# Optimization experiments

Measured on AMD Instinct MI355X. Metric: run time of the kernel, lower is better.

The kernel has to match this reference:

```python
import jax, jax.numpy as jnp
import numpy as np

B, S, D, H = 2, 2048, 1024, 16
HD = D // H  # head_dim = 64


def setup_inputs() -> dict:
    key = jax.random.key(0)
    ks = jax.random.split(key, 5)
    scale = 0.02
    x = jax.random.normal(ks[0], (B, S, D), dtype=jnp.float32)
    Wq = scale * jax.random.normal(ks[1], (H, D, HD), dtype=jnp.float32)
    Wk = scale * jax.random.normal(ks[2], (H, D, HD), dtype=jnp.float32)
    Wv = scale * jax.random.normal(ks[3], (H, D, HD), dtype=jnp.float32)
    Wo = scale * jax.random.normal(ks[4], (D, D), dtype=jnp.float32)
    bq = jnp.zeros((H, HD), dtype=jnp.float32)
    bk = jnp.zeros((H, HD), dtype=jnp.float32)
    bv = jnp.zeros((H, HD), dtype=jnp.float32)
    bo = jnp.zeros((D,), dtype=jnp.float32)
    return {"x": x, "Wq": Wq, "bq": bq, "Wk": Wk, "bk": bk,
            "Wv": Wv, "bv": bv, "Wo": Wo, "bo": bo}


def reference(x, Wq, bq, Wk, bk, Wv, bv, Wo, bo):
    # Per-head QKV projections (the torch module's per-head nn.Linear list,
    # vectorized over the head axis h). Dropout is identity (eval mode).
    q = jnp.einsum("bsd,hde->bhse", x, Wq) + bq[None, :, None, :]  # [B,H,S,HD]
    k = jnp.einsum("bsd,hde->bhse", x, Wk) + bk[None, :, None, :]
    v = jnp.einsum("bsd,hde->bhse", x, Wv) + bv[None, :, None, :]

    norm = jnp.asarray(np.sqrt(HD), dtype=x.dtype)
    scores = jnp.einsum("bhse,bhte->bhst", q, k) / norm  # [B,H,S,S]
    causal = jnp.tril(jnp.ones((S, S), dtype=bool))
    scores = jnp.where(causal[None, None], scores, jnp.asarray(-jnp.inf, dtype=scores.dtype))
    attn = jax.nn.softmax(scores, axis=-1)

    wv = jnp.einsum("bhst,bhte->bhse", attn, v)          # [B,H,S,HD]
    wv = jnp.transpose(wv, (0, 2, 1, 3)).reshape(B, S, D)  # concat heads on last dim
    out = wv @ Wo.T + bo                                   # output projection
    return out
```

## Files before the change

### kernel.cpp

```cpp
#include <hip/hip_runtime.h>


#define DD 1024
#define SS 2048
#define BB 2
#define HH 16
#define HD 64
#define QSCALE 0.18033688011112042f

typedef __attribute__((ext_vector_type(8))) short short8;
typedef __attribute__((ext_vector_type(4))) float float4v;
typedef unsigned short ushort;
typedef unsigned int uint;

__device__ inline ushort f2bf(float f) {
    union { float f; uint i; } v; v.f = f;
    uint r = v.i + 0x7FFF + ((v.i >> 16) & 1);
    return (ushort)(r >> 16);
}
#if __has_builtin(__builtin_amdgcn_cvt_pk_bf16_f32)
typedef __bf16 bf16x2 __attribute__((ext_vector_type(2)));
__device__ inline uint pack_bf2(float a, float b) {
    union { bf16x2 v; uint u; } c;
    c.v = __builtin_amdgcn_cvt_pk_bf16_f32(a, b);
    return c.u;
}
#else
__device__ inline uint pack_bf2(float a, float b) {
    union { float f; uint i; } x, y; x.f = a; y.f = b;
    return ((x.i + 0x8000u) >> 16) | (((y.i + 0x8000u) >> 16) << 16);
}
#endif

__device__ __forceinline__ void cp16(const ushort* g, ushort* l) {
    __builtin_amdgcn_global_load_lds((const __attribute__((address_space(1))) void*)g,
                                     (__attribute__((address_space(3))) void*)l,
                                     16, 0, 0);
}

__global__ __launch_bounds__(256) void prep(const float* __restrict__ x,
                                            const float* __restrict__ Wo,
                                            const float* __restrict__ Wq,
                                            const float* __restrict__ Wk,
                                            const float* __restrict__ Wv,
                                            ushort* __restrict__ xb,
                                            ushort* __restrict__ Wob,
                                            ushort* __restrict__ W3T) {
    __shared__ ushort T[64][65];
    int bid = blockIdx.x, t = threadIdx.x;
    if (bid < 5120) {
        const float* src; ushort* dst; int j;
        if (bid < 4096) { src = x;  dst = xb;  j = bid * 256 + t; }
        else            { src = Wo; dst = Wob; j = (bid - 4096) * 256 + t; }
        float4 v = ((const float4*)src)[j];
        ushort o[4] = { f2bf(v.x), f2bf(v.y), f2bf(v.z), f2bf(v.w) };
        ((uint2*)dst)[j] = *(const uint2*)o;
        return;
    }
    int i = bid - 5120;
    int z = i >> 8, h = (i >> 4) & 15, d0 = (i & 15) * 64;
    const float* W = z == 0 ? Wq : (z == 1 ? Wk : Wv);
    const float* Wh = W + h * DD * HD;
    ushort* Wt = W3T + ((size_t)z * HH + h) * HD * DD;
    #pragma unroll
    for (int s = 0; s < 4; s++) {
        int idx = t + s * 256;
        int d = idx >> 4, e4 = (idx & 15) * 4;
        float4 v = *(const float4*)(Wh + (d0 + d) * HD + e4);
        T[d][e4 + 0] = f2bf(v.x); T[d][e4 + 1] = f2bf(v.y);
        T[d][e4 + 2] = f2bf(v.z); T[d][e4 + 3] = f2bf(v.w);
    }
    __syncthreads();
    #pragma unroll
    for (int s = 0; s < 2; s++) {
        int idx = t + s * 256;
        int e = idx >> 3, d8 = (idx & 7) * 8;
        ushort tmp[8];
        #pragma unroll
        for (int j = 0; j < 8; j++) tmp[j] = T[d8 + j][e];
        *(uint4*)(Wt + e * DD + d0 + d8) = *(uint4*)tmp;
    }
}

__global__ __launch_bounds__(256) void gemm_qkv(const ushort* __restrict__ xb,
                                                const ushort* __restrict__ W3T,
                                                const float* __restrict__ bq,
                                                const float* __restrict__ bk,
                                                const float* __restrict__ bv,
                                                ushort* __restrict__ qb,
                                                ushort* __restrict__ kb,
                                                ushort* __restrict__ vT) {
    __shared__ ushort Al[128 * 64];
    __shared__ ushort Bl[3][64 * 64];
    int m0 = blockIdx.x * 128, n0 = blockIdx.y * 64;
    int t = threadIdx.x, lane = t & 63, w = t >> 6;
    int wm = w & 1, wn = w >> 1;
    int qm = lane >> 4, lm = lane & 15;

    const ushort* W0 = W3T + (size_t)n0 * DD;
    const ushort* W1 = W3T + (size_t)(HH * HD + n0) * DD;
    const ushort* W2 = W3T + (size_t)(2 * HH * HD + n0) * DD;

    float4v acc[3][4][2] = {};
    for (int k0 = 0; k0 < DD; k0 += 64) {
        __syncthreads();
        #pragma unroll
        for (int s = 0; s < 4; s++) {
            int c = t + s * 256;
            int row = c >> 3;
            int j = (c & 7) ^ (row & 7);
            cp16(xb + (size_t)(m0 + row) * DD + k0 + j * 8, Al + c * 8);
        }
        #pragma unroll
        for (int s = 0; s < 2; s++) {
            int c = t + s * 256;
            int row = c >> 3;
            int j = (c & 7) ^ (row & 7);
            cp16(W0 + (size_t)row * DD + k0 + j * 8, Bl[0] + c * 8);
            cp16(W1 + (size_t)row * DD + k0 + j * 8, Bl[1] + c * 8);
            cp16(W2 + (size_t)row * DD + k0 + j * 8, Bl[2] + c * 8);
        }
        __syncthreads();
        #pragma unroll
        for (int h2 = 0; h2 < 2; h2++) {
            int sw = ((((h2 << 2) | qm) ^ (lm & 7)) << 3);
            short8 a[4];
            #pragma unroll
            for (int i = 0; i < 4; i++)
                a[i] = *(const short8*)(Al + ((wm * 64 + i * 16 + lm) << 6) + sw);
            #pragma unroll
            for (int z = 0; z < 3; z++) {
                short8 b0 = *(const short8*)(Bl[z] + ((wn * 32 + lm) << 6) + sw);
                short8 b1 = *(const short8*)(Bl[z] + ((wn * 32 + 16 + lm) << 6) + sw);
                if (z == 2) {
                    #pragma unroll
                    for (int i = 0; i < 4; i++) {
                        acc[2][i][0] = __builtin_amdgcn_mfma_f32_16x16x32_bf16(a[i], b0, acc[2][i][0], 0, 0, 0);
                        acc[2][i][1] = __builtin_amdgcn_mfma_f32_16x16x32_bf16(a[i], b1, acc[2][i][1], 0, 0, 0);
                    }
                } else {
                    #pragma unroll
                    for (int i = 0; i < 4; i++) {
                        acc[z][i][0] = __builtin_amdgcn_mfma_f32_16x16x32_bf16(b0, a[i], acc[z][i][0], 0, 0, 0);
                        acc[z][i][1] = __builtin_amdgcn_mfma_f32_16x16x32_bf16(b1, a[i], acc[z][i][1], 0, 0, 0);
                    }
                }
            }
        }
    }
    #pragma unroll
    for (int z = 0; z < 2; z++) {
        const float* bias = z == 0 ? bq : bk;
        ushort* Out = z == 0 ? qb : kb;
        float sc = z == 0 ? QSCALE : 1.0f;
        #pragma unroll
        for (int j = 0; j < 2; j++) {
            int nb = n0 + wn * 32 + j * 16 + qm * 4;
            float4 b4 = *(const float4*)(bias + nb);
            #pragma unroll
            for (int i = 0; i < 4; i++) {
                int m = m0 + wm * 64 + i * 16 + lm;
                uint2 o2;
                o2.x = pack_bf2((acc[z][i][j][0] + b4.x) * sc, (acc[z][i][j][1] + b4.y) * sc);
                o2.y = pack_bf2((acc[z][i][j][2] + b4.z) * sc, (acc[z][i][j][3] + b4.w) * sc);
                *(uint2*)(Out + (size_t)m * DD + nb) = o2;
            }
        }
    }
    #pragma unroll
    for (int j = 0; j < 2; j++) {
        int n = n0 + wn * 32 + j * 16 + lm;
        int h = n >> 6, e = n & 63;
        float bb = bv[n];
        #pragma unroll
        for (int i = 0; i < 4; i++) {
            int m = m0 + wm * 64 + i * 16 + qm * 4;
            int b_ = m >> 11, s = m & (SS - 1);
            uint2 o2;
            o2.x = pack_bf2(acc[2][i][j][0] + bb, acc[2][i][j][1] + bb);
            o2.y = pack_bf2(acc[2][i][j][2] + bb, acc[2][i][j][3] + bb);
            *(uint2*)(vT + ((size_t)(b_ * HH + h) * HD + e) * SS + s) = o2;
        }
    }
}

__global__ __launch_bounds__(256, 4) void attn(const ushort* __restrict__ Q,
                                               const ushort* __restrict__ K,
                                               const ushort* __restrict__ VT,
                                               ushort* __restrict__ O) {
    __shared__ ushort Ql[64 * 64];
    __shared__ ushort Kl[2][64 * 64];
    __shared__ ushort Vl[2][64 * 64];
    int id = blockIdx.x;
    int bh = id & 31;
    int j5 = (id >> 5) & 7;
    int quad = id >> 8;
    int qt = (quad == 0) ? (31 - j5) : (quad == 1) ? (16 + j5)
           : (quad == 2) ? (15 - j5) : j5;
    int b = bh >> 4, h = bh & 15;
    int m0 = qt * 64;
    const ushort* Qp = Q + (size_t)b * SS * DD + h * HD;
    const ushort* Kp = K + (size_t)b * SS * DD + h * HD;
    const ushort* Vp = VT + (size_t)bh * HD * SS;
    int t = threadIdx.x, lane = t & 63, w = t >> 6;
    int qm = lane >> 4, lm = lane & 15;
    int qg = m0 + w * 16 + lm;
    int swz = ((qm ^ (lm & 7)) << 3);
    int swz1 = (((4 | qm) ^ (lm & 7)) << 3);

    #pragma unroll
    for (int s2 = 0; s2 < 2; s2++) {
        int c = t + s2 * 256;
        int row = c >> 3, sj = (c & 7) ^ (row & 7);
        cp16(Qp + (size_t)(m0 + row) * DD + sj * 8, Ql + c * 8);
        cp16(Kp + (size_t)row * DD + sj * 8, Kl[0] + c * 8);
        cp16(Vp + (size_t)row * SS + sj * 8, Vl[0] + c * 8);
    }
    __syncthreads();

    short8 qf[2];
    qf[0] = *(const short8*)(Ql + ((w * 16 + lm) << 6) + swz);
    qf[1] = *(const short8*)(Ql + ((w * 16 + lm) << 6) + swz1);

    float4v o[4] = {};
    float li = 0.f;
    int cur = 0;

    for (int jt = 0; jt <= qt; jt++) {
        if (jt) __syncthreads();
        if (jt < qt) {
            int nn = (jt + 1) * 64;
            #pragma unroll
            for (int s2 = 0; s2 < 2; s2++) {
                int c = t + s2 * 256;
                int row = c >> 3, sj = (c & 7) ^ (row & 7);
                cp16(Kp + (size_t)(nn + row) * DD + sj * 8, Kl[cur ^ 1] + c * 8);
                cp16(Vp + (size_t)row * SS + nn + sj * 8, Vl[cur ^ 1] + c * 8);
            }
        }

        float4v s[4] = {};
        __builtin_amdgcn_s_setprio(1);
        #pragma unroll
        for (int j = 0; j < 4; j++) {
            short8 ak0 = *(const short8*)(Kl[cur] + ((j * 16 + lm) << 6) + swz);
            short8 ak1 = *(const short8*)(Kl[cur] + ((j * 16 + lm) << 6) + swz1);
            s[j] = __builtin_amdgcn_mfma_f32_16x16x32_bf16(ak0, qf[0], s[j], 0, 0, 0);
            s[j] = __builtin_amdgcn_mfma_f32_16x16x32_bf16(ak1, qf[1], s[j], 0, 0, 0);
        }
        __builtin_amdgcn_s_setprio(0);
        if (jt == qt) {
            #pragma unroll
            for (int j = 0; j < 4; j++)
                #pragma unroll
                for (int r = 0; r < 4; r++)
                    if (jt * 64 + j * 16 + qm * 4 + r > qg) s[j][r] = -__builtin_inff();
        }
        #pragma unroll
        for (int j = 0; j < 4; j++) {
            float p0 = __builtin_amdgcn_exp2f(s[j][0]);
            float p1 = __builtin_amdgcn_exp2f(s[j][1]);
            float p2 = __builtin_amdgcn_exp2f(s[j][2]);
            float p3 = __builtin_amdgcn_exp2f(s[j][3]);
            li += (p0 + p1) + (p2 + p3);
            uint2 u; u.x = pack_bf2(p0, p1); u.y = pack_bf2(p2, p3);
            int pc = (2 * j + (qm >> 1)) ^ (lm & 7);
            *(uint2*)(Ql + ((w * 16 + lm) << 6) + (pc << 3) + (qm & 1) * 4) = u;
        }
        asm volatile("s_waitcnt lgkmcnt(0)" ::: "memory");

        __builtin_amdgcn_s_setprio(1);
        #pragma unroll
        for (int kc = 0; kc < 2; kc++) {
            short8 ap = *(const short8*)(Ql + ((w * 16 + lm) << 6) + (kc ? swz1 : swz));
            #pragma unroll
            for (int jn = 0; jn < 4; jn++) {
                short8 av = *(const short8*)(Vl[cur] + ((jn * 16 + lm) << 6) + (kc ? swz1 : swz));
                o[jn] = __builtin_amdgcn_mfma_f32_16x16x32_bf16(av, ap, o[jn], 0, 0, 0);
            }
        }
        __builtin_amdgcn_s_setprio(0);
        cur ^= 1;
    }
    li += __shfl_xor(li, 16, 64);
    li += __shfl_xor(li, 32, 64);
    float inv = 1.f / li;
    ushort* Ob = O + ((size_t)b * SS + qg) * DD + h * HD;
    #pragma unroll
    for (int jn = 0; jn < 4; jn++) {
        uint2 u;
        u.x = pack_bf2(o[jn][0] * inv, o[jn][1] * inv);
        u.y = pack_bf2(o[jn][2] * inv, o[jn][3] * inv);
        *(uint2*)(Ob + jn * 16 + qm * 4) = u;
    }
}

__global__ __launch_bounds__(256) void gemm_out(const ushort* __restrict__ X,
                                                const ushort* __restrict__ Wob,
                                                const float* __restrict__ bo,
                                                float* __restrict__ Out) {
    __shared__ ushort Al[128 * 64];
    __shared__ ushort Bl[64 * 64];
    int m0 = blockIdx.x * 128, n0 = blockIdx.y * 64;
    int t = threadIdx.x, lane = t & 63, w = t >> 6;
    int wm = w & 1, wn = w >> 1;
    int qm = lane >> 4, lm = lane & 15;

    float4v acc[4][2] = {};
    for (int k0 = 0; k0 < DD; k0 += 64) {
        __syncthreads();
        #pragma unroll
        for (int s = 0; s < 4; s++) {
            int c = t + s * 256;
            int row = c >> 3;
            int j = (c & 7) ^ (row & 7);
            cp16(X + (size_t)(m0 + row) * DD + k0 + j * 8, Al + c * 8);
        }
        #pragma unroll
        for (int s = 0; s < 2; s++) {
            int c = t + s * 256;
            int row = c >> 3;
            int j = (c & 7) ^ (row & 7);
            cp16(Wob + (size_t)(n0 + row) * DD + k0 + j * 8, Bl + c * 8);
        }
        __syncthreads();
        #pragma unroll
        for (int h2 = 0; h2 < 2; h2++) {
            int sw = ((((h2 << 2) | qm) ^ (lm & 7)) << 3);
            short8 a[4], b[2];
            #pragma unroll
            for (int i = 0; i < 4; i++)
                a[i] = *(const short8*)(Al + ((wm * 64 + i * 16 + lm) << 6) + sw);
            #pragma unroll
            for (int j = 0; j < 2; j++)
                b[j] = *(const short8*)(Bl + ((wn * 32 + j * 16 + lm) << 6) + sw);
            #pragma unroll
            for (int i = 0; i < 4; i++)
                #pragma unroll
                for (int j = 0; j < 2; j++)
                    acc[i][j] = __builtin_amdgcn_mfma_f32_16x16x32_bf16(b[j], a[i], acc[i][j], 0, 0, 0);
        }
    }
    #pragma unroll
    for (int j = 0; j < 2; j++) {
        int nb = n0 + wn * 32 + j * 16 + qm * 4;
        float4 b4 = *(const float4*)(bo + nb);
        #pragma unroll
        for (int i = 0; i < 4; i++) {
            int m = m0 + wm * 64 + i * 16 + lm;
            float4 st;
            st.x = acc[i][j][0] + b4.x;
            st.y = acc[i][j][1] + b4.y;
            st.z = acc[i][j][2] + b4.z;
            st.w = acc[i][j][3] + b4.w;
            *(float4*)(Out + (size_t)m * DD + nb) = st;
        }
    }
}

extern "C" void kernel_launch(void* const* d_in, const int* in_sizes, int n_in,
                              void* d_out, int out_size, void* d_ws, size_t ws_size,
                              hipStream_t stream) {
    const float* x   = (const float*)d_in[0];
    const float* Wq  = (const float*)d_in[1];
    const float* bq  = (const float*)d_in[2];
    const float* Wk  = (const float*)d_in[3];
    const float* bk  = (const float*)d_in[4];
    const float* Wv_ = (const float*)d_in[5];
    const float* bv  = (const float*)d_in[6];
    const float* Wo  = (const float*)d_in[7];
    const float* bo  = (const float*)d_in[8];
    float* out = (float*)d_out;

    ushort* xb  = (ushort*)d_ws;
    ushort* W3T = xb  + (size_t)BB * SS * DD;
    ushort* Wob = W3T + (size_t)3 * HH * HD * DD;
    ushort* qb  = Wob + (size_t)DD * DD;
    ushort* kb  = qb + (size_t)BB * SS * DD;
    ushort* vT  = kb + (size_t)BB * SS * DD;
    ushort* wvb = vT + (size_t)BB * SS * DD;

    prep<<<dim3(5888), 256, 0, stream>>>(x, Wo, Wq, Wk, Wv_, xb, Wob, W3T);
    gemm_qkv<<<dim3(32, 16), 256, 0, stream>>>(xb, W3T, bq, bk, bv, qb, kb, vT);
    attn<<<dim3(1024), 256, 0, stream>>>(qb, kb, vT, wvb);
    gemm_out<<<dim3(32, 16), 256, 0, stream>>>(wvb, Wob, bo, out);
}
```

Baseline: 181.3 us.

## Process two query row groups per wave in attention, halving block threads

The attention kernel now runs 2 waves per block instead of 4. Each wave handles 32 query rows as two 16-row groups, so every K and V fragment read from shared memory feeds two MFMAs. This cuts LDS read traffic per MFMA and improves operand reuse. In exchange it uses more registers per wave (launch bounds change to 128 threads, min 2 blocks) and has fewer waves per block to hide the load and sync latency.

After: 187.7 us. 3.5% more time.

```diff
diff --git a/kernel.cpp b/kernel.cpp
--- a/kernel.cpp
+++ b/kernel.cpp
@@ -184,7 +184,7 @@
     }
 }
 
-__global__ __launch_bounds__(256, 4) void attn(const ushort* __restrict__ Q,
+__global__ __launch_bounds__(128, 2) void attn(const ushort* __restrict__ Q,
                                                const ushort* __restrict__ K,
                                                const ushort* __restrict__ VT,
                                                ushort* __restrict__ O) {
@@ -204,13 +204,12 @@
     const ushort* Vp = VT + (size_t)bh * HD * SS;
     int t = threadIdx.x, lane = t & 63, w = t >> 6;
     int qm = lane >> 4, lm = lane & 15;
-    int qg = m0 + w * 16 + lm;
     int swz = ((qm ^ (lm & 7)) << 3);
     int swz1 = (((4 | qm) ^ (lm & 7)) << 3);
 
     #pragma unroll
-    for (int s2 = 0; s2 < 2; s2++) {
-        int c = t + s2 * 256;
+    for (int s2 = 0; s2 < 4; s2++) {
+        int c = t + s2 * 128;
         int row = c >> 3, sj = (c & 7) ^ (row & 7);
         cp16(Qp + (size_t)(m0 + row) * DD + sj * 8, Ql + c * 8);
         cp16(Kp + (size_t)row * DD + sj * 8, Kl[0] + c * 8);
@@ -218,12 +217,16 @@
     }
     __syncthreads();
 
-    short8 qf[2];
-    qf[0] = *(const short8*)(Ql + ((w * 16 + lm) << 6) + swz);
-    qf[1] = *(const short8*)(Ql + ((w * 16 + lm) << 6) + swz1);
-
-    float4v o[4] = {};
-    float li = 0.f;
+    short8 qf[2][2];
+    #pragma unroll
+    for (int g = 0; g < 2; g++) {
+        int rb = (w * 32 + g * 16 + lm) << 6;
+        qf[g][0] = *(const short8*)(Ql + rb + swz);
+        qf[g][1] = *(const short8*)(Ql + rb + swz1);
+    }
+
+    float4v o[4][2] = {};
+    float li[2] = {0.f, 0.f};
     int cur = 0;
 
     for (int jt = 0; jt <= qt; jt++) {
@@ -231,67 +234,88 @@
         if (jt < qt) {
             int nn = (jt + 1) * 64;
             #pragma unroll
-            for (int s2 = 0; s2 < 2; s2++) {
-                int c = t + s2 * 256;
+            for (int s2 = 0; s2 < 4; s2++) {
+                int c = t + s2 * 128;
                 int row = c >> 3, sj = (c & 7) ^ (row & 7);
                 cp16(Kp + (size_t)(nn + row) * DD + sj * 8, Kl[cur ^ 1] + c * 8);
                 cp16(Vp + (size_t)row * SS + nn + sj * 8, Vl[cur ^ 1] + c * 8);
             }
         }
 
-        float4v s[4] = {};
+        float4v s[4][2] = {};
         __builtin_amdgcn_s_setprio(1);
         #pragma unroll
         for (int j = 0; j < 4; j++) {
             short8 ak0 = *(const short8*)(Kl[cur] + ((j * 16 + lm) << 6) + swz);
             short8 ak1 = *(const short8*)(Kl[cur] + ((j * 16 + lm) << 6) + swz1);
-            s[j] = __builtin_amdgcn_mfma_f32_16x16x32_bf16(ak0, qf[0], s[j], 0, 0, 0);
-            s[j] = __builtin_amdgcn_mfma_f32_16x16x32_bf16(ak1, qf[1], s[j], 0, 0, 0);
+            #pragma unroll
+            for (int g = 0; g < 2; g++) {
+                s[j][g] = __builtin_amdgcn_mfma_f32_16x16x32_bf16(ak0, qf[g][0], s[j][g], 0, 0, 0);
+                s[j][g] = __builtin_amdgcn_mfma_f32_16x16x32_bf16(ak1, qf[g][1], s[j][g], 0, 0, 0);
+            }
         }
         __builtin_amdgcn_s_setprio(0);
         if (jt == qt) {
             #pragma unroll
-            for (int j = 0; j < 4; j++)
+            for (int g = 0; g < 2; g++) {
+                int qg = m0 + w * 32 + g * 16 + lm;
                 #pragma unroll
-                for (int r = 0; r < 4; r++)
-                    if (jt * 64 + j * 16 + qm * 4 + r > qg) s[j][r] = -__builtin_inff();
-        }
-        #pragma unroll
-        for (int j = 0; j < 4; j++) {
-            float p0 = __builtin_amdgcn_exp2f(s[j][0]);
-            float p1 = __builtin_amdgcn_exp2f(s[j][1]);
-            float p2 = __builtin_amdgcn_exp2f(s[j][2]);
-            float p3 = __builtin_amdgcn_exp2f(s[j][3]);
-            li += (p0 + p1) + (p2 + p3);
-            uint2 u; u.x = pack_bf2(p0, p1); u.y = pack_bf2(p2, p3);
-            int pc = (2 * j + (qm >> 1)) ^ (lm & 7);
-            *(uint2*)(Ql + ((w * 16 + lm) << 6) + (pc << 3) + (qm & 1) * 4) = u;
+                for (int j = 0; j < 4; j++)
+                    #pragma unroll
+                    for (int r = 0; r < 4; r++)
+                        if (jt * 64 + j * 16 + qm * 4 + r > qg) s[j][g][r] = -__builtin_inff();
+            }
+        }
+        #pragma unroll
+        for (int g = 0; g < 2; g++) {
+            int rb = (w * 32 + g * 16 + lm) << 6;
+            #pragma unroll
+            for (int j = 0; j < 4; j++) {
+                float p0 = __builtin_amdgcn_exp2f(s[j][g][0]);
+                float p1 = __builtin_amdgcn_exp2f(s[j][g][1]);
+                float p2 = __builtin_amdgcn_exp2f(s[j][g][2]);
+                float p3 = __builtin_amdgcn_exp2f(s[j][g][3]);
+                li[g] += (p0 + p1) + (p2 + p3);
+                uint2 u; u.x = pack_bf2(p0, p1); u.y = pack_bf2(p2, p3);
+                int pc = (2 * j + (qm >> 1)) ^ (lm & 7);
+                *(uint2*)(Ql + rb + (pc << 3) + (qm & 1) * 4) = u;
+            }
         }
         asm volatile("s_waitcnt lgkmcnt(0)" ::: "memory");
 
         __builtin_amdgcn_s_setprio(1);
         #pragma unroll
         for (int kc = 0; kc < 2; kc++) {
-            short8 ap = *(const short8*)(Ql + ((w * 16 + lm) << 6) + (kc ? swz1 : swz));
+            short8 ap[2];
+            #pragma unroll
+            for (int g = 0; g < 2; g++)
+                ap[g] = *(const short8*)(Ql + ((w * 32 + g * 16 + lm) << 6) + (kc ? swz1 : swz));
             #pragma unroll
             for (int jn = 0; jn < 4; jn++) {
                 short8 av = *(const short8*)(Vl[cur] + ((jn * 16 + lm) << 6) + (kc ? swz1 : swz));
-                o[jn] = __builtin_amdgcn_mfma_f32_16x16x32_bf16(av, ap, o[jn], 0, 0, 0);
+                #pragma unroll
+                for (int g = 0; g < 2; g++)
+                    o[jn][g] = __builtin_amdgcn_mfma_f32_16x16x32_bf16(av, ap[g], o[jn][g], 0, 0, 0);
             }
         }
         __builtin_amdgcn_s_setprio(0);
         cur ^= 1;
     }
-    li += __shfl_xor(li, 16, 64);
-    li += __shfl_xor(li, 32, 64);
-    float inv = 1.f / li;
-    ushort* Ob = O + ((size_t)b * SS + qg) * DD + h * HD;
-    #pragma unroll
-    for (int jn = 0; jn < 4; jn++) {
-        uint2 u;
-        u.x = pack_bf2(o[jn][0] * inv, o[jn][1] * inv);
-        u.y = pack_bf2(o[jn][2] * inv, o[jn][3] * inv);
-        *(uint2*)(Ob + jn * 16 + qm * 4) = u;
+    #pragma unroll
+    for (int g = 0; g < 2; g++) {
+        float l = li[g];
+        l += __shfl_xor(l, 16, 64);
+        l += __shfl_xor(l, 32, 64);
+        float inv = 1.f / l;
+        int qg = m0 + w * 32 + g * 16 + lm;
+        ushort* Ob = O + ((size_t)b * SS + qg) * DD + h * HD;
+        #pragma unroll
+        for (int jn = 0; jn < 4; jn++) {
+            uint2 u;
+            u.x = pack_bf2(o[jn][g][0] * inv, o[jn][g][1] * inv);
+            u.y = pack_bf2(o[jn][g][2] * inv, o[jn][g][3] * inv);
+            *(uint2*)(Ob + jn * 16 + qm * 4) = u;
+        }
     }
 }
 
@@ -382,6 +406,6 @@
 
     prep<<<dim3(5888), 256, 0, stream>>>(x, Wo, Wq, Wk, Wv_, xb, Wob, W3T);
     gemm_qkv<<<dim3(32, 16), 256, 0, stream>>>(xb, W3T, bq, bk, bv, qb, kb, vT);
-    attn<<<dim3(1024), 256, 0, stream>>>(qb, kb, vT, wvb);
+    attn<<<dim3(1024), 128, 0, stream>>>(qb, kb, vT, wvb);
     gemm_out<<<dim3(32, 16), 256, 0, stream>>>(wvb, Wob, bo, out);
 }
```

## Rework attention with 32x32 MFMA, register-resident P, and split-KV wave pairs

Applied to the files above, without the earlier changes.

The attention kernel switches from 16x16x32 to 32x32x16 MFMA tiles. The P fragment is kept in registers via permlane32 swaps instead of being round-tripped through LDS. The two wave pairs each process alternating KV tiles, and their partial outputs and row sums are reduced through LDS at the end. This removes the LDS write/read of P and raises MFMA work per instruction. In exchange it adds a final cross-wave reduction, only half the waves do the epilogue, and the causal load balance across wave pairs becomes uneven.

Result: faster. 170.9 us, median of 2 (-5.7%).

```diff
diff --git a/kernel.cpp b/kernel.cpp
--- a/kernel.cpp
+++ b/kernel.cpp
@@ -10,6 +10,8 @@
 
 typedef __attribute__((ext_vector_type(8))) short short8;
 typedef __attribute__((ext_vector_type(4))) float float4v;
+typedef __attribute__((ext_vector_type(16))) float f32x16;
+typedef __attribute__((ext_vector_type(4))) uint uint4v;
 typedef unsigned short ushort;
 typedef unsigned int uint;
 
@@ -29,6 +31,26 @@
 __device__ inline uint pack_bf2(float a, float b) {
     union { float f; uint i; } x, y; x.f = a; y.f = b;
     return ((x.i + 0x8000u) >> 16) | (((y.i + 0x8000u) >> 16) << 16);
+}
+#endif
+
+__device__ inline short8 u4_to_s8(uint4v u) {
+    union { uint4v u; short8 s; } cv; cv.u = u; return cv.s;
+}
+
+#if __has_builtin(__builtin_amdgcn_permlane32_swap)
+typedef unsigned uint2v __attribute__((ext_vector_type(2)));
+__device__ inline void pl32_swap(uint& d, uint& s) {
+    uint2v r = __builtin_amdgcn_permlane32_swap(d, s, false, false);
+    d = r[0]; s = r[1];
+}
+#else
+__device__ inline void pl32_swap(uint& d, uint& s) {
+    uint dx = __shfl_xor(d, 32, 64), sx = __shfl_xor(s, 32, 64);
+    bool hi = (threadIdx.x & 32) != 0;
+    uint nd = hi ? sx : d;
+    uint ns = hi ? s : dx;
+    d = nd; s = ns;
 }
 #endif
 
@@ -188,9 +210,7 @@
                                                const ushort* __restrict__ K,
                                                const ushort* __restrict__ VT,
                                                ushort* __restrict__ O) {
-    __shared__ ushort Ql[64 * 64];
-    __shared__ ushort Kl[2][64 * 64];
-    __shared__ ushort Vl[2][64 * 64];
+    __shared__ ushort LB[20480];
     int id = blockIdx.x;
     int bh = id & 31;
     int j5 = (id >> 5) & 7;
@@ -203,95 +223,151 @@
     const ushort* Kp = K + (size_t)b * SS * DD + h * HD;
     const ushort* Vp = VT + (size_t)bh * HD * SS;
     int t = threadIdx.x, lane = t & 63, w = t >> 6;
-    int qm = lane >> 4, lm = lane & 15;
-    int qg = m0 + w * 16 + lm;
-    int swz = ((qm ^ (lm & 7)) << 3);
-    int swz1 = (((4 | qm) ^ (lm & 7)) << 3);
-
-    #pragma unroll
-    for (int s2 = 0; s2 < 2; s2++) {
-        int c = t + s2 * 256;
-        int row = c >> 3, sj = (c & 7) ^ (row & 7);
-        cp16(Qp + (size_t)(m0 + row) * DD + sj * 8, Ql + c * 8);
-        cp16(Kp + (size_t)row * DD + sj * 8, Kl[0] + c * 8);
-        cp16(Vp + (size_t)row * SS + sj * 8, Vl[0] + c * 8);
+    int pr = w >> 1, wq = w & 1;
+    int ln = lane & 31, hi = lane >> 5;
+    int c0 = t, c1 = t + 256;
+    int r0 = c0 >> 3, s0 = (c0 & 7) ^ (r0 & 7);
+    int r1 = c1 >> 3, s1 = (c1 & 7) ^ (r1 & 7);
+
+    cp16(Qp + (size_t)(m0 + r0) * DD + s0 * 8, LB + c0 * 8);
+    cp16(Qp + (size_t)(m0 + r1) * DD + s1 * 8, LB + c1 * 8);
+    cp16(Kp + (size_t)r0 * DD + s0 * 8, LB + 4096 + c0 * 8);
+    cp16(Kp + (size_t)r1 * DD + s1 * 8, LB + 4096 + c1 * 8);
+    cp16(Vp + (size_t)r0 * SS + s0 * 8, LB + 8192 + c0 * 8);
+    cp16(Vp + (size_t)r1 * SS + s1 * 8, LB + 8192 + c1 * 8);
+    if (qt >= 1) {
+        cp16(Kp + (size_t)(64 + r0) * DD + s0 * 8, LB + 12288 + c0 * 8);
+        cp16(Kp + (size_t)(64 + r1) * DD + s1 * 8, LB + 12288 + c1 * 8);
+        cp16(Vp + (size_t)r0 * SS + 64 + s0 * 8, LB + 16384 + c0 * 8);
+        cp16(Vp + (size_t)r1 * SS + 64 + s1 * 8, LB + 16384 + c1 * 8);
     }
     __syncthreads();
 
-    short8 qf[2];
-    qf[0] = *(const short8*)(Ql + ((w * 16 + lm) << 6) + swz);
-    qf[1] = *(const short8*)(Ql + ((w * 16 + lm) << 6) + swz1);
-
-    float4v o[4] = {};
+    short8 qf[4];
+    int qrow = wq * 32 + ln;
+    #pragma unroll
+    for (int ds_ = 0; ds_ < 4; ds_++)
+        qf[ds_] = *(const short8*)(LB + (qrow << 6) + ((((ds_ << 1) | hi) ^ (qrow & 7)) << 3));
+
+    ushort* Kb = LB + 4096 + pr * 8192;
+    ushort* Vb = LB + 8192 + pr * 8192;
+    f32x16 o[2] = {};
     float li = 0.f;
-    int cur = 0;
-
-    for (int jt = 0; jt <= qt; jt++) {
-        if (jt) __syncthreads();
-        if (jt < qt) {
-            int nn = (jt + 1) * 64;
-            #pragma unroll
-            for (int s2 = 0; s2 < 2; s2++) {
-                int c = t + s2 * 256;
-                int row = c >> 3, sj = (c & 7) ^ (row & 7);
-                cp16(Kp + (size_t)(nn + row) * DD + sj * 8, Kl[cur ^ 1] + c * 8);
-                cp16(Vp + (size_t)row * SS + nn + sj * 8, Vl[cur ^ 1] + c * 8);
-            }
-        }
-
-        float4v s[4] = {};
-        __builtin_amdgcn_s_setprio(1);
-        #pragma unroll
-        for (int j = 0; j < 4; j++) {
-            short8 ak0 = *(const short8*)(Kl[cur] + ((j * 16 + lm) << 6) + swz);
-            short8 ak1 = *(const short8*)(Kl[cur] + ((j * 16 + lm) << 6) + swz1);
-            s[j] = __builtin_amdgcn_mfma_f32_16x16x32_bf16(ak0, qf[0], s[j], 0, 0, 0);
-            s[j] = __builtin_amdgcn_mfma_f32_16x16x32_bf16(ak1, qf[1], s[j], 0, 0, 0);
-        }
-        __builtin_amdgcn_s_setprio(0);
-        if (jt == qt) {
-            #pragma unroll
-            for (int j = 0; j < 4; j++)
+    int nss = (qt + 2) >> 1;
+
+    for (int ss = 0; ss < nss; ss++) {
+        int myjt = 2 * ss + pr;
+        if (myjt <= qt) {
+            #pragma unroll
+            for (int kt = 0; kt < 2; kt++) {
+                f32x16 sacc = {};
+                __builtin_amdgcn_s_setprio(1);
                 #pragma unroll
-                for (int r = 0; r < 4; r++)
-                    if (jt * 64 + j * 16 + qm * 4 + r > qg) s[j][r] = -__builtin_inff();
-        }
-        #pragma unroll
-        for (int j = 0; j < 4; j++) {
-            float p0 = __builtin_amdgcn_exp2f(s[j][0]);
-            float p1 = __builtin_amdgcn_exp2f(s[j][1]);
-            float p2 = __builtin_amdgcn_exp2f(s[j][2]);
-            float p3 = __builtin_amdgcn_exp2f(s[j][3]);
-            li += (p0 + p1) + (p2 + p3);
-            uint2 u; u.x = pack_bf2(p0, p1); u.y = pack_bf2(p2, p3);
-            int pc = (2 * j + (qm >> 1)) ^ (lm & 7);
-            *(uint2*)(Ql + ((w * 16 + lm) << 6) + (pc << 3) + (qm & 1) * 4) = u;
-        }
-        asm volatile("s_waitcnt lgkmcnt(0)" ::: "memory");
-
-        __builtin_amdgcn_s_setprio(1);
-        #pragma unroll
-        for (int kc = 0; kc < 2; kc++) {
-            short8 ap = *(const short8*)(Ql + ((w * 16 + lm) << 6) + (kc ? swz1 : swz));
-            #pragma unroll
-            for (int jn = 0; jn < 4; jn++) {
-                short8 av = *(const short8*)(Vl[cur] + ((jn * 16 + lm) << 6) + (kc ? swz1 : swz));
-                o[jn] = __builtin_amdgcn_mfma_f32_16x16x32_bf16(av, ap, o[jn], 0, 0, 0);
-            }
-        }
-        __builtin_amdgcn_s_setprio(0);
-        cur ^= 1;
-    }
-    li += __shfl_xor(li, 16, 64);
-    li += __shfl_xor(li, 32, 64);
-    float inv = 1.f / li;
-    ushort* Ob = O + ((size_t)b * SS + qg) * DD + h * HD;
-    #pragma unroll
-    for (int jn = 0; jn < 4; jn++) {
-        uint2 u;
-        u.x = pack_bf2(o[jn][0] * inv, o[jn][1] * inv);
-        u.y = pack_bf2(o[jn][2] * inv, o[jn][3] * inv);
-        *(uint2*)(Ob + jn * 16 + qm * 4) = u;
+                for (int ds_ = 0; ds_ < 4; ds_++) {
+                    int row = kt * 32 + ln;
+                    short8 ak = *(const short8*)(Kb + (row << 6) + ((((ds_ << 1) | hi) ^ (row & 7)) << 3));
+                    sacc = __builtin_amdgcn_mfma_f32_32x32x16_bf16(ak, qf[ds_], sacc, 0, 0, 0);
+                }
+                __builtin_amdgcn_s_setprio(0);
+                if (myjt == qt) {
+                    #pragma unroll
+                    for (int r = 0; r < 16; r++) {
+                        int kk = kt * 32 + (r & 3) + 8 * (r >> 2) + 4 * hi;
+                        if (kk > qrow) sacc[r] = -__builtin_inff();
+                    }
+                }
+                float p[16];
+                #pragma unroll
+                for (int r = 0; r < 16; r++) {
+                    p[r] = __builtin_amdgcn_exp2f(sacc[r]);
+                    li += p[r];
+                }
+                uint4v pw[2];
+                #pragma unroll
+                for (int ks = 0; ks < 2; ks++) {
+                    uint c01 = pack_bf2(p[ks * 8 + 0], p[ks * 8 + 1]);
+                    uint c23 = pack_bf2(p[ks * 8 + 2], p[ks * 8 + 3]);
+                    uint c45 = pack_bf2(p[ks * 8 + 4], p[ks * 8 + 5]);
+                    uint c67 = pack_bf2(p[ks * 8 + 6], p[ks * 8 + 7]);
+                    pl32_swap(c01, c45);
+                    pl32_swap(c23, c67);
+                    uint4v pv; pv[0] = c01; pv[1] = c23; pv[2] = c45; pv[3] = c67;
+                    pw[ks] = pv;
+                }
+                __builtin_amdgcn_s_setprio(1);
+                #pragma unroll
+                for (int et = 0; et < 2; et++) {
+                    #pragma unroll
+                    for (int ks = 0; ks < 2; ks++) {
+                        int row = et * 32 + ln;
+                        int ch = ((kt << 2) | (ks << 1) | hi) ^ (row & 7);
+                        short8 av = *(const short8*)(Vb + (row << 6) + (ch << 3));
+                        o[et] = __builtin_amdgcn_mfma_f32_32x32x16_bf16(av, u4_to_s8(pw[ks]), o[et], 0, 0, 0);
+                    }
+                }
+                __builtin_amdgcn_s_setprio(0);
+            }
+        }
+        __syncthreads();
+        int nx = 2 * ss + 2;
+        if (nx <= qt) {
+            cp16(Kp + (size_t)(nx * 64 + r0) * DD + s0 * 8, LB + 4096 + c0 * 8);
+            cp16(Kp + (size_t)(nx * 64 + r1) * DD + s1 * 8, LB + 4096 + c1 * 8);
+            cp16(Vp + (size_t)r0 * SS + nx * 64 + s0 * 8, LB + 8192 + c0 * 8);
+            cp16(Vp + (size_t)r1 * SS + nx * 64 + s1 * 8, LB + 8192 + c1 * 8);
+        }
+        if (nx + 1 <= qt) {
+            cp16(Kp + (size_t)((nx + 1) * 64 + r0) * DD + s0 * 8, LB + 12288 + c0 * 8);
+            cp16(Kp + (size_t)((nx + 1) * 64 + r1) * DD + s1 * 8, LB + 12288 + c1 * 8);
+            cp16(Vp + (size_t)r0 * SS + (nx + 1) * 64 + s0 * 8, LB + 16384 + c0 * 8);
+            cp16(Vp + (size_t)r1 * SS + (nx + 1) * 64 + s1 * 8, LB + 16384 + c1 * 8);
+        }
+        __syncthreads();
+    }
+
+    float* cb = (float*)(LB + 4096);
+    float* cl = (float*)(LB + 12288);
+    if (pr == 1) {
+        float* dst = cb + ((size_t)(wq * 64 + lane)) * 32;
+        #pragma unroll
+        for (int et = 0; et < 2; et++)
+            #pragma unroll
+            for (int g2 = 0; g2 < 4; g2++) {
+                int slot = et * 4 + g2;
+                float4v v4;
+                v4[0] = o[et][g2 * 4 + 0]; v4[1] = o[et][g2 * 4 + 1];
+                v4[2] = o[et][g2 * 4 + 2]; v4[3] = o[et][g2 * 4 + 3];
+                *(float4v*)(dst + ((slot ^ (lane & 7)) << 2)) = v4;
+            }
+        cl[wq * 64 + lane] = li;
+    }
+    __syncthreads();
+    if (pr == 0) {
+        float* src = cb + ((size_t)(wq * 64 + lane)) * 32;
+        #pragma unroll
+        for (int et = 0; et < 2; et++)
+            #pragma unroll
+            for (int g2 = 0; g2 < 4; g2++) {
+                int slot = et * 4 + g2;
+                float4v v4 = *(const float4v*)(src + ((slot ^ (lane & 7)) << 2));
+                o[et][g2 * 4 + 0] += v4[0]; o[et][g2 * 4 + 1] += v4[1];
+                o[et][g2 * 4 + 2] += v4[2]; o[et][g2 * 4 + 3] += v4[3];
+            }
+        li += cl[wq * 64 + lane];
+        li += __shfl_xor(li, 32, 64);
+        float inv = 1.f / li;
+        int qg = m0 + wq * 32 + ln;
+        ushort* Ob = O + ((size_t)b * SS + qg) * DD + h * HD;
+        #pragma unroll
+        for (int et = 0; et < 2; et++)
+            #pragma unroll
+            for (int g2 = 0; g2 < 4; g2++) {
+                int ec = et * 32 + g2 * 8 + hi * 4;
+                uint2 u;
+                u.x = pack_bf2(o[et][g2 * 4 + 0] * inv, o[et][g2 * 4 + 1] * inv);
+                u.y = pack_bf2(o[et][g2 * 4 + 2] * inv, o[et][g2 * 4 + 3] * inv);
+                *(uint2*)(Ob + ec) = u;
+            }
     }
 }
 
```
